# Performance work log

Measured on AMD Instinct MI355X. Metric: run time of the kernel, lower is better.

## Reference

```python
import jax, jax.numpy as jnp
import numpy as np

D_MODEL = 256
N_HEADS = 8
HEAD_DIM = D_MODEL // N_HEADS  # 32
N_LEVELS = 4
N_POINTS = 4
LEVEL_SHAPES = [(100, 100), (50, 50), (25, 25), (13, 13)]
LEVEL_STARTS = [0] + list(np.cumsum([h * w for h, w in LEVEL_SHAPES]))[:-1]
LEN_IN = int(sum(h * w for h, w in LEVEL_SHAPES))  # 13294
BATCH = 2
LEN_Q = LEN_IN  # encoder self-attention


def _offset_bias():
    # faithful to MSDeformAttn._reset_parameters for sampling_offsets bias
    thetas = np.arange(N_HEADS, dtype=np.float32) * (2.0 * np.pi / N_HEADS)
    grid = np.stack([np.cos(thetas), np.sin(thetas)], -1)
    grid = grid / np.abs(grid).max(-1, keepdims=True)
    grid = np.tile(grid.reshape(N_HEADS, 1, 1, 2), (1, N_LEVELS, N_POINTS, 1))
    for i in range(N_POINTS):
        grid[:, :, i, :] *= i + 1
    return jnp.asarray(grid.reshape(-1), dtype=jnp.float32)


def setup_inputs() -> dict:
    key = jax.random.key(0)
    ks = jax.random.split(key, 10)
    s = 1.0 / np.sqrt(D_MODEL)
    inp = {
        "query": jax.random.normal(ks[0], (BATCH, LEN_Q, D_MODEL), jnp.float32),
        "reference_points": jax.random.uniform(ks[1], (BATCH, LEN_Q, N_LEVELS, 2), jnp.float32),
        "input_flatten": jax.random.normal(ks[2], (BATCH, LEN_IN, D_MODEL), jnp.float32),
        "input_spatial_shapes": jnp.asarray(LEVEL_SHAPES, dtype=jnp.int32),
        "W_value": jax.random.normal(ks[3], (D_MODEL, D_MODEL), jnp.float32) * s,
        "b_value": jnp.zeros((D_MODEL,), jnp.float32),
        "W_off": jax.random.normal(ks[4], (D_MODEL, N_HEADS * N_LEVELS * N_POINTS * 2), jnp.float32) * 0.01,
        "b_off": _offset_bias(),
        "W_attn": jax.random.normal(ks[5], (D_MODEL, N_HEADS * N_LEVELS * N_POINTS), jnp.float32) * 0.01,
        "b_attn": jnp.zeros((N_HEADS * N_LEVELS * N_POINTS,), jnp.float32),
        "W_out": jax.random.normal(ks[6], (D_MODEL, D_MODEL), jnp.float32) * s,
        "b_out": jnp.zeros((D_MODEL,), jnp.float32),
    }
    return inp


def _corner(v_t, ix, iy, h, w):
    # v_t: (n, M, h*w, D); ix/iy: (n, M, LqP) int32. Zero padding outside.
    valid = (ix >= 0) & (ix < w) & (iy >= 0) & (iy < h)
    idx = jnp.clip(iy, 0, h - 1) * w + jnp.clip(ix, 0, w - 1)
    g = jnp.take_along_axis(v_t, idx[..., None], axis=2)  # (n, M, LqP, D)
    return g * valid[..., None].astype(v_t.dtype)


def _ms_deform_attn(query, reference_points, input_flatten,
                    W_value, b_value, W_off, b_off, W_attn, b_attn, W_out, b_out):
    n, lq, _ = query.shape
    value = (input_flatten @ W_value + b_value).reshape(n, LEN_IN, N_HEADS, HEAD_DIM)
    offs = (query @ W_off + b_off).reshape(n, lq, N_HEADS, N_LEVELS, N_POINTS, 2)
    aw = jax.nn.softmax(
        (query @ W_attn + b_attn).reshape(n, lq, N_HEADS, N_LEVELS * N_POINTS), axis=-1
    ).reshape(n, lq, N_HEADS, N_LEVELS, N_POINTS)
    # offset_normalizer = (w, h) per level
    norm = jnp.asarray([[w, h] for h, w in LEVEL_SHAPES], dtype=query.dtype)
    loc = reference_points[:, :, None, :, None, :] + offs / norm[None, None, None, :, None, :]

    acc = jnp.zeros((n, N_HEADS, lq, HEAD_DIM), dtype=value.dtype)
    for l, (h, w) in enumerate(LEVEL_SHAPES):
        s0 = LEVEL_STARTS[l]
        v_t = jnp.transpose(value[:, s0:s0 + h * w], (0, 2, 1, 3))  # (n, M, hw, D)
        ll = loc[:, :, :, l]  # (n, lq, M, P, 2) in [0,1]
        # grid_sample bilinear, align_corners=False: pixel = coord*size - 0.5
        x = ll[..., 0] * w - 0.5
        y = ll[..., 1] * h - 0.5
        x0 = jnp.floor(x); y0 = jnp.floor(y)
        tx = x - x0; ty = y - y0
        ix0 = x0.astype(jnp.int32); iy0 = y0.astype(jnp.int32)
        flat = lambda a: jnp.transpose(a, (0, 2, 1, 3)).reshape(n, N_HEADS, lq * N_POINTS)
        ix0f, iy0f = flat(ix0), flat(iy0)
        txf = flat(tx)[..., None]; tyf = flat(ty)[..., None]
        g00 = _corner(v_t, ix0f, iy0f, h, w)
        g01 = _corner(v_t, ix0f + 1, iy0f, h, w)
        g10 = _corner(v_t, ix0f, iy0f + 1, h, w)
        g11 = _corner(v_t, ix0f + 1, iy0f + 1, h, w)
        samp = (g00 * (1 - txf) * (1 - tyf) + g01 * txf * (1 - tyf)
                + g10 * (1 - txf) * tyf + g11 * txf * tyf)
        samp = samp.reshape(n, N_HEADS, lq, N_POINTS, HEAD_DIM)
        wl = jnp.transpose(aw[:, :, :, l], (0, 2, 1, 3))[..., None]  # (n, M, lq, P, 1)
        acc = acc + (samp * wl).sum(axis=3)

    out = jnp.transpose(acc, (0, 2, 1, 3)).reshape(n, lq, D_MODEL)
    return out @ W_out + b_out


def reference(query, reference_points, input_flatten, input_spatial_shapes,
              W_value, b_value, W_off, b_off, W_attn, b_attn, W_out, b_out):
    # input_spatial_shapes carried for signature fidelity; level geometry is static.
    return _ms_deform_attn(query, reference_points, input_flatten,
                           W_value, b_value, W_off, b_off, W_attn, b_attn, W_out, b_out)
```

## Files before the change

kernel.cpp:

```cpp
#include <hip/hip_runtime.h>

#define NH 8
#define HD 32
#define NL 4
#define NP 4
#define DM 256
#define LEN_IN_C 13294
#define LQ_C 13294
#define B_C 2
#define M_TOTAL (B_C * LQ_C)
#define MT_TILES 1662
#define RT32_TILES 831
#define GQ 32
#define QBLKS 831

typedef __attribute__((ext_vector_type(8))) short short8;
typedef __attribute__((ext_vector_type(4))) float floatx4;

__device__ __forceinline__ unsigned short f2bf(float x) {
    union { float f; unsigned int u; } a; a.f = x;
    unsigned int r = (a.u + 0x7FFFu + ((a.u >> 16) & 1u)) >> 16;
    return (unsigned short)r;
}
__device__ __forceinline__ unsigned short f2h(float x) {
    unsigned int r;
    asm("v_cvt_f16_f32 %0, %1" : "=v"(r) : "v"(x));
    return (unsigned short)r;
}
__device__ __forceinline__ unsigned int cvtpk_bf16(float lo, float hi) {
    unsigned int r;
    asm("v_cvt_pk_bf16_f32 %0, %1, %2" : "=v"(r) : "v"(lo), "v"(hi));
    return r;
}

#define FMAMIX_LO(acc, v, w) \
    asm("v_fma_mix_f32 %0, %1, %2, %0 op_sel_hi:[1,0,0]" : "+v"(acc) : "v"(v), "v"(w))
#define FMAMIX_HI(acc, v, w) \
    asm("v_fma_mix_f32 %0, %1, %2, %0 op_sel:[1,0,0] op_sel_hi:[1,0,0]" : "+v"(acc) : "v"(v), "v"(w))

__device__ __forceinline__ void conv_b_body(const float* __restrict__ W,
                                            unsigned short* __restrict__ Bsw,
                                            int Nsrc, int NTsrc, int NTtotal, int ntOff,
                                            int vblk) {
    const int u = vblk * 256 + threadIdx.x;
    const int lane = u & 63;
    const int unit = u >> 6;
    const int ntl = unit % NTsrc;
    const int kc = unit / NTsrc;
    const int n = ntl * 16 + (lane & 15);
    const int k0 = kc * 32 + (lane >> 4) * 8;
    short8 v;
#pragma unroll
    for (int j = 0; j < 8; ++j)
        v[j] = (short)f2bf(W[(size_t)(k0 + j) * Nsrc + n]);
    ((short8*)Bsw)[(size_t)(kc * NTtotal + ntOff + ntl) * 64 + lane] = v;
}

__global__ __launch_bounds__(256) void conv_weights_kernel(const float* __restrict__ Wv,
                                                           const float* __restrict__ Woff,
                                                           const float* __restrict__ Wattn,
                                                           const float* __restrict__ Wout,
                                                           const float* __restrict__ boff,
                                                           const float* __restrict__ battn,
                                                           unsigned short* __restrict__ BswV,
                                                           unsigned short* __restrict__ BswOA,
                                                           unsigned short* __restrict__ BswO,
                                                           float* __restrict__ fbias,
                                                           unsigned short* __restrict__ value,
                                                           unsigned short* __restrict__ AccSw) {
    const int blk = blockIdx.x;
    if (blk < 32)        conv_b_body(Wv,    BswV,  256, 16, 16, 0,  blk);
    else if (blk < 64)   conv_b_body(Woff,  BswOA, 256, 16, 24, 0,  blk - 32);
    else if (blk < 80)   conv_b_body(Wattn, BswOA, 128,  8, 24, 16, blk - 64);
    else if (blk < 112)  conv_b_body(Wout,  BswO,  256, 16, 16, 0,  blk - 80);
    else if (blk < 114) {
        const int t = (blk - 112) * 256 + threadIdx.x;
        if (t < 384) fbias[t] = (t < 256) ? boff[t] : battn[t - 256];
        else if (t < 416) {
            const int j = t - 384;
            value[-32 + j] = 0;
            value[(size_t)M_TOTAL * 256 + j] = 0;
        }
    } else {
        const int idx = threadIdx.x;
        if (idx < 128) {
            const int kc = idx >> 4;
            const int sub = idx & 15;
            const int lane = (12 + (sub & 3)) + 16 * (sub >> 2);
            const size_t unit = (size_t)(1661 * 8 + kc) * 64 + lane;
            short8 z = (short8){0, 0, 0, 0, 0, 0, 0, 0};
            ((short8*)AccSw)[unit] = z;
        }
    }
}

template <int NT, int OUTMODE>
__device__ __forceinline__ void gemm_lds_pipe(unsigned short* __restrict__ sA,
                                              const float* __restrict__ A,
                                              const unsigned short* __restrict__ Bsw,
                                              const float* __restrict__ bias,
                                              void* __restrict__ Cout, int M, int rt32) {
    constexpr int NTW = NT / 4;
    const int tid = threadIdx.x;
    const int lane = tid & 63;
    const int wave = tid >> 6;
    const int trow = rt32 * 32;

#pragma unroll
    for (int i = 0; i < 8; ++i) {
        const int li = i * 1024 + tid * 4;
        const int lrow = li >> 8;
        const int lcol = li & 255;
        const int srow = min(trow + lrow, M - 1);
        const float4 f = *(const float4*)(A + (size_t)srow * 256 + lcol);
        uint2 pk;
        pk.x = cvtpk_bf16(f.x, f.y);
        pk.y = cvtpk_bf16(f.z, f.w);
        const int lb = (li * 2) ^ ((lrow & 7) << 4);
        *(uint2*)((char*)sA + lb) = pk;
    }
    __syncthreads();

    const int m = lane & 15;
    const int q = lane >> 4;
    const short8* Bu = (const short8*)Bsw;
    const int swz = (m & 7) << 4;

    floatx4 acc[2][NTW];
#pragma unroll
    for (int r = 0; r < 2; ++r)
#pragma unroll
        for (int t = 0; t < NTW; ++t) acc[r][t] = (floatx4){0.f, 0.f, 0.f, 0.f};

    short8 br[2][NTW];
    short8 ar[2][2];
#pragma unroll
    for (int t = 0; t < NTW; ++t)
        br[0][t] = Bu[(size_t)(0 * NT + wave * NTW + t) * 64 + lane];
    ar[0][0] = *(const short8*)((const char*)sA + ((m * 512 + 0 * 64 + q * 16) ^ swz));
    ar[0][1] = *(const short8*)((const char*)sA + (((m + 16) * 512 + 0 * 64 + q * 16) ^ swz));

#pragma unroll
    for (int kc = 0; kc < 8; ++kc) {
        const int cur = kc & 1;
        const int nxt = cur ^ 1;
        if (kc < 7) {
#pragma unroll
            for (int t = 0; t < NTW; ++t)
                br[nxt][t] = Bu[(size_t)((kc + 1) * NT + wave * NTW + t) * 64 + lane];
            ar[nxt][0] = *(const short8*)((const char*)sA + ((m * 512 + (kc + 1) * 64 + q * 16) ^ swz));
            ar[nxt][1] = *(const short8*)((const char*)sA + (((m + 16) * 512 + (kc + 1) * 64 + q * 16) ^ swz));
        }
#pragma unroll
        for (int t = 0; t < NTW; ++t) {
            acc[0][t] = __builtin_amdgcn_mfma_f32_16x16x32_bf16(ar[cur][0], br[cur][t], acc[0][t], 0, 0, 0);
            acc[1][t] = __builtin_amdgcn_mfma_f32_16x16x32_bf16(ar[cur][1], br[cur][t], acc[1][t], 0, 0, 0);
        }
    }

    const int N = NT * 16;
    const int colq = lane & 15;
    const int rowq = (lane >> 4) * 4;
#pragma unroll
    for (int t = 0; t < NTW; ++t) {
        const int col = (wave * NTW + t) * 16 + colq;
        const float bc = bias[col];
#pragma unroll
        for (int r = 0; r < 2; ++r) {
#pragma unroll
            for (int reg = 0; reg < 4; ++reg) {
                const int row = trow + r * 16 + rowq + reg;
                if (row < M) {
                    const float v = acc[r][t][reg] + bc;
                    if (OUTMODE == 1) {
                        const int bb = row >= LEN_IN_C;
                        const int pos = row - (bb ? LEN_IN_C : 0);
                        const int hh = col >> 5;
                        const int dd = col & 31;
                        ((unsigned short*)Cout)[((size_t)((bb << 3) + hh) * LEN_IN_C + pos) * 32 + dd] = f2h(v);
                    } else {
                        ((float*)Cout)[(size_t)row * N + col] = v;
                    }
                }
            }
        }
    }
}

__global__ __launch_bounds__(256) void front_gemm_kernel(const float* __restrict__ inflat,
                                                         const float* __restrict__ query,
                                                         const unsigned short* __restrict__ BswV,
                                                         const unsigned short* __restrict__ BswOA,
                                                         const float* __restrict__ bv,
                                                         const float* __restrict__ fbias,
                                                         unsigned short* __restrict__ value,
                                                         float* __restrict__ fused, int M) {
    __shared__ unsigned short sA[32 * 256];
    const int x = blockIdx.x;
    const int rt32 = x >> 1;
    if ((x & 1) == 0)
        gemm_lds_pipe<16, 1>(sA, inflat, BswV, bv, (void*)value, M, rt32);
    else
        gemm_lds_pipe<24, 0>(sA, query, BswOA, fbias, (void*)fused, M, rt32);
}

__global__ __launch_bounds__(256) void back_gemm_kernel(const unsigned short* __restrict__ Asw,
                                                        const unsigned short* __restrict__ Bsw,
                                                        const float* __restrict__ bias,
                                                        float* __restrict__ Cout, int M) {
    constexpr int NT = 16;
    constexpr int NTW = 4;
    const int tid = threadIdx.x;
    const int lane = tid & 63;
    const int wave = tid >> 6;
    const int rt0 = blockIdx.x * 2;

    const short8* Au = (const short8*)Asw;
    const short8* Bu = (const short8*)Bsw;

    floatx4 acc[2][NTW];
#pragma unroll
    for (int r = 0; r < 2; ++r)
#pragma unroll
        for (int t = 0; t < NTW; ++t) acc[r][t] = (floatx4){0.f, 0.f, 0.f, 0.f};

    short8 br[2][NTW];
    short8 ar[2][2];
#pragma unroll
    for (int t = 0; t < NTW; ++t)
        br[0][t] = Bu[(size_t)(0 * NT + wave * NTW + t) * 64 + lane];
    ar[0][0] = Au[(size_t)(rt0 * 8 + 0) * 64 + lane];
    ar[0][1] = Au[(size_t)((rt0 + 1) * 8 + 0) * 64 + lane];

#pragma unroll
    for (int kc = 0; kc < 8; ++kc) {
        const int cur = kc & 1;
        const int nxt = cur ^ 1;
        if (kc < 7) {
#pragma unroll
            for (int t = 0; t < NTW; ++t)
                br[nxt][t] = Bu[(size_t)((kc + 1) * NT + wave * NTW + t) * 64 + lane];
            ar[nxt][0] = Au[(size_t)(rt0 * 8 + kc + 1) * 64 + lane];
            ar[nxt][1] = Au[(size_t)((rt0 + 1) * 8 + kc + 1) * 64 + lane];
        }
#pragma unroll
        for (int t = 0; t < NTW; ++t) {
            acc[0][t] = __builtin_amdgcn_mfma_f32_16x16x32_bf16(ar[cur][0], br[cur][t], acc[0][t], 0, 0, 0);
            acc[1][t] = __builtin_amdgcn_mfma_f32_16x16x32_bf16(ar[cur][1], br[cur][t], acc[1][t], 0, 0, 0);
        }
    }

    const int colq = lane & 15;
    const int rowq = (lane >> 4) * 4;
#pragma unroll
    for (int t = 0; t < NTW; ++t) {
        const int col = (wave * NTW + t) * 16 + colq;
        const float bc = bias[col];
#pragma unroll
        for (int r = 0; r < 2; ++r) {
#pragma unroll
            for (int reg = 0; reg < 4; ++reg) {
                const int row = (rt0 + r) * 16 + rowq + reg;
                if (row < M)
                    Cout[(size_t)row * 256 + col] = acc[r][t][reg] + bc;
            }
        }
    }
}

__global__ __launch_bounds__(256, 4) void msda_sample_kernel(const float* __restrict__ refp,
                                                             const unsigned short* __restrict__ value,
                                                             const float* __restrict__ fused,
                                                             unsigned short* __restrict__ AccSw) {
    constexpr int lvl_hw[4] = {100, 50, 25, 13};
    constexpr int lvl_s[4] = {0, 10000, 12500, 13125};

    const int wg = blockIdx.x;
    const int h = wg & 7;
    const int q0 = (wg >> 3) * GQ;
    const int tid = threadIdx.x;

    __shared__ float s_ref[GQ * 8];
    __shared__ uint4 s_pd[2][GQ * 17];

    s_ref[tid] = refp[min(q0 * 8 + tid, M_TOTAL * 8 - 1)];
    __syncthreads();

#pragma unroll
    for (int jj = 0; jj < 2; ++jj) {
        const int job = jj * 256 + tid;
        const int qq = job >> 4;
        const int t16 = job & 15;
        const int l = t16 >> 2;
        const int bq = min(q0 + qq, M_TOTAL - 1);
        const int b = (bq >= LQ_C) ? 1 : 0;

        const float logit = fused[(size_t)bq * 384 + 256 + h * 16 + t16];
        float m = logit;
#pragma unroll
        for (int mask = 1; mask < 16; mask <<= 1) m = fmaxf(m, __shfl_xor(m, mask));
        const float e = expf(logit - m);
        float s = e;
#pragma unroll
        for (int mask = 1; mask < 16; mask <<= 1) s += __shfl_xor(s, mask);
        const float aw = e / s;

        const int whl = lvl_hw[l];
        const float fwh = (float)whl;
        const float2 oxy = *(const float2*)(fused + (size_t)bq * 384 + (h * 16 + t16) * 2);
        const float x = s_ref[qq * 8 + l * 2] * fwh + oxy.x - 0.5f;
        const float y = s_ref[qq * 8 + l * 2 + 1] * fwh + oxy.y - 0.5f;
        const float x0f = floorf(x), y0f = floorf(y);
        const float tx = x - x0f, ty = y - y0f;
        const int ix0 = (int)x0f, iy0 = (int)y0f;

        const bool xv0 = (unsigned)ix0 < (unsigned)whl;
        const bool xv1 = (unsigned)(ix0 + 1) < (unsigned)whl;
        const bool yv0 = (unsigned)iy0 < (unsigned)whl;
        const bool yv1 = (unsigned)(iy0 + 1) < (unsigned)whl;

        const int cxp = min(max(ix0, -1), whl - 1);
        const int cy0 = min(max(iy0, 0), whl - 1);
        const int cy1 = min(max(iy0 + 1, 0), whl - 1);

        const int posb = (b * 8 + h) * LEN_IN_C + lvl_s[l];
        const int offT = (posb + cy0 * whl + cxp) * 64;
        const int offB = (posb + cy1 * whl + cxp) * 64;
        const float w00 = (xv0 && yv0) ? aw * (1.f - tx) * (1.f - ty) : 0.f;
        const float w01 = (xv1 && yv0) ? aw * tx * (1.f - ty) : 0.f;
        const float w10 = (xv0 && yv1) ? aw * (1.f - tx) * ty : 0.f;
        const float w11 = (xv1 && yv1) ? aw * tx * ty : 0.f;
        const int slot = qq * 17 + t16;
        uint4 d0, d1;
        d0.x = (unsigned)offT; d0.y = (unsigned)offB;
        d0.z = __float_as_uint(w00); d0.w = __float_as_uint(w10);
        d1.x = (unsigned)offT; d1.y = (unsigned)offB;
        d1.z = __float_as_uint(w01); d1.w = __float_as_uint(w11);
        s_pd[0][slot] = d0;
        s_pd[1][slot] = d1;
    }
    __syncthreads();

    const int qq = tid >> 3;
    const int l8 = tid & 7;
    const char* vbp = (const char*)value + l8 * 16;
    const int side = (l8 >> 2) & 1;
    const uint4* pd = &s_pd[side][qq * 17];

    uint4 dsc[2][4];
    uint4 vt[2][4], vb[2][4];
#pragma unroll
    for (int j = 0; j < 4; ++j) dsc[0][j] = pd[j];
#pragma unroll
    for (int j = 0; j < 4; ++j) {
        vt[0][j] = *(const uint4*)(vbp + (int)dsc[0][j].x);
        vb[0][j] = *(const uint4*)(vbp + (int)dsc[0][j].y);
    }

    float a0 = 0.f, a1 = 0.f, a2 = 0.f, a3 = 0.f;
    float a4 = 0.f, a5 = 0.f, a6 = 0.f, a7 = 0.f;
#pragma unroll
    for (int c = 0; c < 4; ++c) {
        const int cur = c & 1;
        const int nxt = cur ^ 1;
        if (c < 3) {
#pragma unroll
            for (int j = 0; j < 4; ++j) dsc[nxt][j] = pd[(c + 1) * 4 + j];
#pragma unroll
            for (int j = 0; j < 4; ++j) {
                vt[nxt][j] = *(const uint4*)(vbp + (int)dsc[nxt][j].x);
                vb[nxt][j] = *(const uint4*)(vbp + (int)dsc[nxt][j].y);
            }
        }
#pragma unroll
        for (int j = 0; j < 4; ++j) {
            const float wt = __uint_as_float(dsc[cur][j].z);
            const float wb = __uint_as_float(dsc[cur][j].w);
            const uint4 t4 = vt[cur][j];
            const uint4 b4 = vb[cur][j];
            FMAMIX_LO(a0, t4.x, wt); FMAMIX_HI(a1, t4.x, wt);
            FMAMIX_LO(a2, t4.y, wt); FMAMIX_HI(a3, t4.y, wt);
            FMAMIX_LO(a4, t4.z, wt); FMAMIX_HI(a5, t4.z, wt);
            FMAMIX_LO(a6, t4.w, wt); FMAMIX_HI(a7, t4.w, wt);
            FMAMIX_LO(a0, b4.x, wb); FMAMIX_HI(a1, b4.x, wb);
            FMAMIX_LO(a2, b4.y, wb); FMAMIX_HI(a3, b4.y, wb);
            FMAMIX_LO(a4, b4.z, wb); FMAMIX_HI(a5, b4.z, wb);
            FMAMIX_LO(a6, b4.w, wb); FMAMIX_HI(a7, b4.w, wb);
        }
    }

    a0 += __shfl_xor(a0, 4); a1 += __shfl_xor(a1, 4);
    a2 += __shfl_xor(a2, 4); a3 += __shfl_xor(a3, 4);
    a4 += __shfl_xor(a4, 4); a5 += __shfl_xor(a5, 4);
    a6 += __shfl_xor(a6, 4); a7 += __shfl_xor(a7, 4);

    const int bq = q0 + qq;
    if (side == 0 && bq < M_TOTAL) {
        const int rt = bq >> 4, mm = bq & 15;
        const int unit = (rt * 8 + h) * 64 + ((l8 & 3) * 16 + mm);
        uint4 o;
        o.x = cvtpk_bf16(a0, a1);
        o.y = cvtpk_bf16(a2, a3);
        o.z = cvtpk_bf16(a4, a5);
        o.w = cvtpk_bf16(a6, a7);
        *(uint4*)(AccSw + (size_t)unit * 8) = o;
    }
}

extern "C" void kernel_launch(void* const* d_in, const int* in_sizes, int n_in,
                              void* d_out, int out_size, void* d_ws, size_t ws_size,
                              hipStream_t stream) {
    const float* query  = (const float*)d_in[0];
    const float* refp   = (const float*)d_in[1];
    const float* inflat = (const float*)d_in[2];
    const float* Wv    = (const float*)d_in[4];
    const float* bv    = (const float*)d_in[5];
    const float* Woff  = (const float*)d_in[6];
    const float* boff  = (const float*)d_in[7];
    const float* Wattn = (const float*)d_in[8];
    const float* battn = (const float*)d_in[9];
    const float* Wout  = (const float*)d_in[10];
    const float* bout  = (const float*)d_in[11];
    float* out = (float*)d_out;

    char* p = (char*)d_ws;
    unsigned short* AccSw = (unsigned short*)p;
    p += (size_t)MT_TILES * 8 * 64 * 8 * sizeof(unsigned short);
    unsigned short* BswV = (unsigned short*)p;   p += (size_t)8 * 16 * 64 * 8 * 2;
    unsigned short* BswOA = (unsigned short*)p;  p += (size_t)8 * 24 * 64 * 8 * 2;
    unsigned short* BswO = (unsigned short*)p;   p += (size_t)8 * 16 * 64 * 8 * 2;
    float* fbias = (float*)p;                    p += 384 * sizeof(float);
    unsigned short* value = (unsigned short*)p + 32;
    p += ((size_t)M_TOTAL * 256 + 64) * sizeof(unsigned short);
    float* fused = (float*)p;                    p += (size_t)M_TOTAL * 384 * 4;

    const int M = M_TOTAL;

    conv_weights_kernel<<<115, 256, 0, stream>>>(Wv, Woff, Wattn, Wout, boff, battn,
                                                 BswV, BswOA, BswO, fbias, value, AccSw);
    front_gemm_kernel<<<RT32_TILES * 2, 256, 0, stream>>>(inflat, query, BswV, BswOA,
                                                          bv, fbias, value, fused, M);
    msda_sample_kernel<<<QBLKS * 8, 256, 0, stream>>>(refp, value, fused, AccSw);
    back_gemm_kernel<<<RT32_TILES, 256, 0, stream>>>(AccSw, BswO, bout, out, M);
}
```

Measured before the change: 198.3 us.

## Make front and back GEMMs persistent with double-buffered prefetch

Both projection GEMMs become persistent grids of 512 blocks that loop over row tiles. The front GEMM double-buffers its LDS staging so the next tile's global loads overlap the current tile's MFMA work. The back GEMM loads the whole weight fragment into registers once per block and ping-pongs A fragments for 16-row tiles. This removes per-tile launch and weight reload cost, at the price of higher register pressure and fewer blocks to hide latency.

Result: slower. 255.4 us (+28.8%).

```diff
diff --git a/kernel.cpp b/kernel.cpp
--- a/kernel.cpp
+++ b/kernel.cpp
@@ -13,6 +13,9 @@
 #define RT32_TILES 831
 #define GQ 32
 #define QBLKS 831
+#define FRONT_BLOCKS 512
+#define FRONT_STRIDE 256
+#define BACK_BLOCKS 512
 
 typedef __attribute__((ext_vector_type(8))) short short8;
 typedef __attribute__((ext_vector_type(4))) float floatx4;
@@ -94,37 +97,42 @@
     }
 }
 
-template <int NT, int OUTMODE>
-__device__ __forceinline__ void gemm_lds_pipe(unsigned short* __restrict__ sA,
-                                              const float* __restrict__ A,
-                                              const unsigned short* __restrict__ Bsw,
-                                              const float* __restrict__ bias,
-                                              void* __restrict__ Cout, int M, int rt32) {
-    constexpr int NTW = NT / 4;
-    const int tid = threadIdx.x;
-    const int lane = tid & 63;
-    const int wave = tid >> 6;
-    const int trow = rt32 * 32;
-
+__device__ __forceinline__ void stage_load(float4 (&stg)[8], const float* __restrict__ A,
+                                           int trow, int M, int tid) {
 #pragma unroll
     for (int i = 0; i < 8; ++i) {
         const int li = i * 1024 + tid * 4;
         const int lrow = li >> 8;
         const int lcol = li & 255;
         const int srow = min(trow + lrow, M - 1);
-        const float4 f = *(const float4*)(A + (size_t)srow * 256 + lcol);
+        stg[i] = *(const float4*)(A + (size_t)srow * 256 + lcol);
+    }
+}
+
+__device__ __forceinline__ void stage_write(unsigned short* sbuf, const float4 (&stg)[8], int tid) {
+#pragma unroll
+    for (int i = 0; i < 8; ++i) {
+        const int li = i * 1024 + tid * 4;
+        const int lrow = li >> 8;
         uint2 pk;
-        pk.x = cvtpk_bf16(f.x, f.y);
-        pk.y = cvtpk_bf16(f.z, f.w);
-        const int lb = (li * 2) ^ ((lrow & 7) << 4);
-        *(uint2*)((char*)sA + lb) = pk;
-    }
-    __syncthreads();
-
+        pk.x = cvtpk_bf16(stg[i].x, stg[i].y);
+        pk.y = cvtpk_bf16(stg[i].z, stg[i].w);
+        *(uint2*)((char*)sbuf + ((li * 2) ^ ((lrow & 7) << 4))) = pk;
+    }
+}
+
+template <int NT, int OUTMODE>
+__device__ __forceinline__ void tile_compute(const unsigned short* sbuf,
+                                             const unsigned short* __restrict__ Bsw,
+                                             const float* __restrict__ bias,
+                                             void* __restrict__ Cout, int M, int rt32,
+                                             int lane, int wave) {
+    constexpr int NTW = NT / 4;
     const int m = lane & 15;
     const int q = lane >> 4;
     const short8* Bu = (const short8*)Bsw;
     const int swz = (m & 7) << 4;
+    const int trow = rt32 * 32;
 
     floatx4 acc[2][NTW];
 #pragma unroll
@@ -137,8 +145,8 @@
 #pragma unroll
     for (int t = 0; t < NTW; ++t)
         br[0][t] = Bu[(size_t)(0 * NT + wave * NTW + t) * 64 + lane];
-    ar[0][0] = *(const short8*)((const char*)sA + ((m * 512 + 0 * 64 + q * 16) ^ swz));
-    ar[0][1] = *(const short8*)((const char*)sA + (((m + 16) * 512 + 0 * 64 + q * 16) ^ swz));
+    ar[0][0] = *(const short8*)((const char*)sbuf + ((m * 512 + 0 * 64 + q * 16) ^ swz));
+    ar[0][1] = *(const short8*)((const char*)sbuf + (((m + 16) * 512 + 0 * 64 + q * 16) ^ swz));
 
 #pragma unroll
     for (int kc = 0; kc < 8; ++kc) {
@@ -148,8 +156,8 @@
 #pragma unroll
             for (int t = 0; t < NTW; ++t)
                 br[nxt][t] = Bu[(size_t)((kc + 1) * NT + wave * NTW + t) * 64 + lane];
-            ar[nxt][0] = *(const short8*)((const char*)sA + ((m * 512 + (kc + 1) * 64 + q * 16) ^ swz));
-            ar[nxt][1] = *(const short8*)((const char*)sA + (((m + 16) * 512 + (kc + 1) * 64 + q * 16) ^ swz));
+            ar[nxt][0] = *(const short8*)((const char*)sbuf + ((m * 512 + (kc + 1) * 64 + q * 16) ^ swz));
+            ar[nxt][1] = *(const short8*)((const char*)sbuf + (((m + 16) * 512 + (kc + 1) * 64 + q * 16) ^ swz));
         }
 #pragma unroll
         for (int t = 0; t < NTW; ++t) {
@@ -187,84 +195,107 @@
     }
 }
 
-__global__ __launch_bounds__(256) void front_gemm_kernel(const float* __restrict__ inflat,
-                                                         const float* __restrict__ query,
-                                                         const unsigned short* __restrict__ BswV,
-                                                         const unsigned short* __restrict__ BswOA,
-                                                         const float* __restrict__ bv,
-                                                         const float* __restrict__ fbias,
-                                                         unsigned short* __restrict__ value,
-                                                         float* __restrict__ fused, int M) {
-    __shared__ unsigned short sA[32 * 256];
-    const int x = blockIdx.x;
-    const int rt32 = x >> 1;
-    if ((x & 1) == 0)
-        gemm_lds_pipe<16, 1>(sA, inflat, BswV, bv, (void*)value, M, rt32);
-    else
-        gemm_lds_pipe<24, 0>(sA, query, BswOA, fbias, (void*)fused, M, rt32);
-}
-
-__global__ __launch_bounds__(256) void back_gemm_kernel(const unsigned short* __restrict__ Asw,
-                                                        const unsigned short* __restrict__ Bsw,
-                                                        const float* __restrict__ bias,
-                                                        float* __restrict__ Cout, int M) {
-    constexpr int NT = 16;
-    constexpr int NTW = 4;
+__global__ __launch_bounds__(256, 2) void front_gemm_kernel(const float* __restrict__ inflat,
+                                                            const float* __restrict__ query,
+                                                            const unsigned short* __restrict__ BswV,
+                                                            const unsigned short* __restrict__ BswOA,
+                                                            const float* __restrict__ bv,
+                                                            const float* __restrict__ fbias,
+                                                            unsigned short* __restrict__ value,
+                                                            float* __restrict__ fused, int M) {
+    __shared__ unsigned short sA[2][32 * 256];
     const int tid = threadIdx.x;
     const int lane = tid & 63;
     const int wave = tid >> 6;
-    const int rt0 = blockIdx.x * 2;
-
+    const int flavor = blockIdx.x & 1;
+    const int rt0 = blockIdx.x >> 1;
+    const float* A = flavor ? query : inflat;
+
+    float4 stg[8];
+    stage_load(stg, A, rt0 * 32, M, tid);
+    stage_write(sA[0], stg, tid);
+
+    int cur = 0;
+    for (int rt = rt0; rt < RT32_TILES; rt += FRONT_STRIDE) {
+        __syncthreads();
+        const int rtn = rt + FRONT_STRIDE;
+        if (rtn < RT32_TILES) stage_load(stg, A, rtn * 32, M, tid);
+        if (flavor == 0)
+            tile_compute<16, 1>(sA[cur], BswV, bv, (void*)value, M, rt, lane, wave);
+        else
+            tile_compute<24, 0>(sA[cur], BswOA, fbias, (void*)fused, M, rt, lane, wave);
+        if (rtn < RT32_TILES) stage_write(sA[cur ^ 1], stg, tid);
+        cur ^= 1;
+    }
+}
+
+__device__ __forceinline__ void back_loadA(short8 (&ar)[8], const short8* __restrict__ Au,
+                                           int rt, int lane) {
+#pragma unroll
+    for (int kc = 0; kc < 8; ++kc)
+        ar[kc] = Au[(size_t)(rt * 8 + kc) * 64 + lane];
+}
+
+__device__ __forceinline__ void back_compute(const short8 (&ar)[8], const short8 (&br)[8][4],
+                                             const float* __restrict__ bias,
+                                             float* __restrict__ Cout, int M, int rt,
+                                             int lane, int wave) {
+    floatx4 acc[4];
+#pragma unroll
+    for (int t = 0; t < 4; ++t) acc[t] = (floatx4){0.f, 0.f, 0.f, 0.f};
+#pragma unroll
+    for (int kc = 0; kc < 8; ++kc)
+#pragma unroll
+        for (int t = 0; t < 4; ++t)
+            acc[t] = __builtin_amdgcn_mfma_f32_16x16x32_bf16(ar[kc], br[kc][t], acc[t], 0, 0, 0);
+
+    const int colq = lane & 15;
+    const int rowq = (lane >> 4) * 4;
+#pragma unroll
+    for (int t = 0; t < 4; ++t) {
+        const int col = (wave * 4 + t) * 16 + colq;
+        const float bc = bias[col];
+#pragma unroll
+        for (int reg = 0; reg < 4; ++reg) {
+            const int row = rt * 16 + rowq + reg;
+            if (row < M)
+                Cout[(size_t)row * 256 + col] = acc[t][reg] + bc;
+        }
+    }
+}
+
+__global__ __launch_bounds__(256, 2) void back_gemm_kernel(const unsigned short* __restrict__ Asw,
+                                                           const unsigned short* __restrict__ Bsw,
+                                                           const float* __restrict__ bias,
+                                                           float* __restrict__ Cout, int M) {
+    const int tid = threadIdx.x;
+    const int lane = tid & 63;
+    const int wave = tid >> 6;
     const short8* Au = (const short8*)Asw;
     const short8* Bu = (const short8*)Bsw;
 
-    floatx4 acc[2][NTW];
-#pragma unroll
-    for (int r = 0; r < 2; ++r)
-#pragma unroll
-        for (int t = 0; t < NTW; ++t) acc[r][t] = (floatx4){0.f, 0.f, 0.f, 0.f};
-
-    short8 br[2][NTW];
-    short8 ar[2][2];
-#pragma unroll
-    for (int t = 0; t < NTW; ++t)
-        br[0][t] = Bu[(size_t)(0 * NT + wave * NTW + t) * 64 + lane];
-    ar[0][0] = Au[(size_t)(rt0 * 8 + 0) * 64 + lane];
-    ar[0][1] = Au[(size_t)((rt0 + 1) * 8 + 0) * 64 + lane];
-
-#pragma unroll
-    for (int kc = 0; kc < 8; ++kc) {
-        const int cur = kc & 1;
-        const int nxt = cur ^ 1;
-        if (kc < 7) {
-#pragma unroll
-            for (int t = 0; t < NTW; ++t)
-                br[nxt][t] = Bu[(size_t)((kc + 1) * NT + wave * NTW + t) * 64 + lane];
-            ar[nxt][0] = Au[(size_t)(rt0 * 8 + kc + 1) * 64 + lane];
-            ar[nxt][1] = Au[(size_t)((rt0 + 1) * 8 + kc + 1) * 64 + lane];
-        }
-#pragma unroll
-        for (int t = 0; t < NTW; ++t) {
-            acc[0][t] = __builtin_amdgcn_mfma_f32_16x16x32_bf16(ar[cur][0], br[cur][t], acc[0][t], 0, 0, 0);
-            acc[1][t] = __builtin_amdgcn_mfma_f32_16x16x32_bf16(ar[cur][1], br[cur][t], acc[1][t], 0, 0, 0);
-        }
-    }
-
-    const int colq = lane & 15;
-    const int rowq = (lane >> 4) * 4;
-#pragma unroll
-    for (int t = 0; t < NTW; ++t) {
-        const int col = (wave * NTW + t) * 16 + colq;
-        const float bc = bias[col];
-#pragma unroll
-        for (int r = 0; r < 2; ++r) {
-#pragma unroll
-            for (int reg = 0; reg < 4; ++reg) {
-                const int row = (rt0 + r) * 16 + rowq + reg;
-                if (row < M)
-                    Cout[(size_t)row * 256 + col] = acc[r][t][reg] + bc;
-            }
-        }
+    short8 br[8][4];
+#pragma unroll
+    for (int kc = 0; kc < 8; ++kc)
+#pragma unroll
+        for (int t = 0; t < 4; ++t)
+            br[kc][t] = Bu[(size_t)(kc * 16 + wave * 4 + t) * 64 + lane];
+
+    short8 arA[8], arB[8];
+    int rt = blockIdx.x;
+    if (rt >= MT_TILES) return;
+    back_loadA(arA, Au, rt, lane);
+    while (true) {
+        int rtn = rt + BACK_BLOCKS;
+        if (rtn < MT_TILES) back_loadA(arB, Au, rtn, lane);
+        back_compute(arA, br, bias, Cout, M, rt, lane, wave);
+        rt = rtn;
+        if (rt >= MT_TILES) break;
+        rtn = rt + BACK_BLOCKS;
+        if (rtn < MT_TILES) back_loadA(arA, Au, rtn, lane);
+        back_compute(arB, br, bias, Cout, M, rt, lane, wave);
+        rt = rtn;
+        if (rt >= MT_TILES) break;
     }
 }
 
@@ -438,8 +469,8 @@
 
     conv_weights_kernel<<<115, 256, 0, stream>>>(Wv, Woff, Wattn, Wout, boff, battn,
                                                  BswV, BswOA, BswO, fbias, value, AccSw);
-    front_gemm_kernel<<<RT32_TILES * 2, 256, 0, stream>>>(inflat, query, BswV, BswOA,
-                                                          bv, fbias, value, fused, M);
+    front_gemm_kernel<<<FRONT_BLOCKS, 256, 0, stream>>>(inflat, query, BswV, BswOA,
+                                                        bv, fbias, value, fused, M);
     msda_sample_kernel<<<QBLKS * 8, 256, 0, stream>>>(refp, value, fused, AccSw);
-    back_gemm_kernel<<<RT32_TILES, 256, 0, stream>>>(AccSw, BswO, bout, out, M);
-}
+    back_gemm_kernel<<<BACK_BLOCKS, 256, 0, stream>>>(AccSw, BswO, bout, out, M);
+}
```

## Stage fp32 A tiles via direct global-to-LDS loads and convert at fragment read

Applied to the files above, without the earlier changes.

The front GEMM no longer loads A through registers and packs it to bf16 in swizzled LDS. It now issues global_load_lds DMA of fp32 rows into padded LDS (row stride 1040 bytes) and converts to bf16 when the MFMA fragments are read. Both front and back GEMMs also drop the explicit register double-buffering of A/B fragments in favour of a plain loop unrolled by 2. This cuts VGPR staging and load instructions, but doubles LDS footprint and traffic and moves the conversion work into the inner loop.

Result: faster. 189.2 us (-4.6%).

```diff
diff --git a/kernel.cpp b/kernel.cpp
--- a/kernel.cpp
+++ b/kernel.cpp
@@ -13,6 +13,7 @@
 #define RT32_TILES 831
 #define GQ 32
 #define QBLKS 831
+#define LROWB 1040
 
 typedef __attribute__((ext_vector_type(8))) short short8;
 typedef __attribute__((ext_vector_type(4))) float floatx4;
@@ -37,6 +38,12 @@
     asm("v_fma_mix_f32 %0, %1, %2, %0 op_sel_hi:[1,0,0]" : "+v"(acc) : "v"(v), "v"(w))
 #define FMAMIX_HI(acc, v, w) \
     asm("v_fma_mix_f32 %0, %1, %2, %0 op_sel:[1,0,0] op_sel_hi:[1,0,0]" : "+v"(acc) : "v"(v), "v"(w))
+
+__device__ __forceinline__ void dma16(const float* g, float* l) {
+    __builtin_amdgcn_global_load_lds(
+        (const __attribute__((address_space(1))) unsigned int*)(g),
+        (__attribute__((address_space(3))) unsigned int*)(l), 16, 0, 0);
+}
 
 __device__ __forceinline__ void conv_b_body(const float* __restrict__ W,
                                             unsigned short* __restrict__ Bsw,
@@ -95,36 +102,15 @@
 }
 
 template <int NT, int OUTMODE>
-__device__ __forceinline__ void gemm_lds_pipe(unsigned short* __restrict__ sA,
-                                              const float* __restrict__ A,
-                                              const unsigned short* __restrict__ Bsw,
-                                              const float* __restrict__ bias,
-                                              void* __restrict__ Cout, int M, int rt32) {
+__device__ __forceinline__ void tile_compute_f32lds(const float* __restrict__ sA,
+                                                    const unsigned short* __restrict__ Bsw,
+                                                    const float* __restrict__ bias,
+                                                    void* __restrict__ Cout, int M, int trow,
+                                                    int lane, int wave) {
     constexpr int NTW = NT / 4;
-    const int tid = threadIdx.x;
-    const int lane = tid & 63;
-    const int wave = tid >> 6;
-    const int trow = rt32 * 32;
-
-#pragma unroll
-    for (int i = 0; i < 8; ++i) {
-        const int li = i * 1024 + tid * 4;
-        const int lrow = li >> 8;
-        const int lcol = li & 255;
-        const int srow = min(trow + lrow, M - 1);
-        const float4 f = *(const float4*)(A + (size_t)srow * 256 + lcol);
-        uint2 pk;
-        pk.x = cvtpk_bf16(f.x, f.y);
-        pk.y = cvtpk_bf16(f.z, f.w);
-        const int lb = (li * 2) ^ ((lrow & 7) << 4);
-        *(uint2*)((char*)sA + lb) = pk;
-    }
-    __syncthreads();
-
     const int m = lane & 15;
     const int q = lane >> 4;
     const short8* Bu = (const short8*)Bsw;
-    const int swz = (m & 7) << 4;
 
     floatx4 acc[2][NTW];
 #pragma unroll
@@ -132,29 +118,24 @@
 #pragma unroll
         for (int t = 0; t < NTW; ++t) acc[r][t] = (floatx4){0.f, 0.f, 0.f, 0.f};
 
-    short8 br[2][NTW];
-    short8 ar[2][2];
-#pragma unroll
-    for (int t = 0; t < NTW; ++t)
-        br[0][t] = Bu[(size_t)(0 * NT + wave * NTW + t) * 64 + lane];
-    ar[0][0] = *(const short8*)((const char*)sA + ((m * 512 + 0 * 64 + q * 16) ^ swz));
-    ar[0][1] = *(const short8*)((const char*)sA + (((m + 16) * 512 + 0 * 64 + q * 16) ^ swz));
-
-#pragma unroll
+#pragma unroll 2
     for (int kc = 0; kc < 8; ++kc) {
-        const int cur = kc & 1;
-        const int nxt = cur ^ 1;
-        if (kc < 7) {
-#pragma unroll
-            for (int t = 0; t < NTW; ++t)
-                br[nxt][t] = Bu[(size_t)((kc + 1) * NT + wave * NTW + t) * 64 + lane];
-            ar[nxt][0] = *(const short8*)((const char*)sA + ((m * 512 + (kc + 1) * 64 + q * 16) ^ swz));
-            ar[nxt][1] = *(const short8*)((const char*)sA + (((m + 16) * 512 + (kc + 1) * 64 + q * 16) ^ swz));
+        short8 a[2];
+#pragma unroll
+        for (int r = 0; r < 2; ++r) {
+            const char* fb = (const char*)sA + (m + r * 16) * LROWB + kc * 128 + q * 32;
+            const float4 f0 = *(const float4*)fb;
+            const float4 f1 = *(const float4*)(fb + 16);
+            union { uint4 u; short8 s; } c;
+            c.u.x = cvtpk_bf16(f0.x, f0.y); c.u.y = cvtpk_bf16(f0.z, f0.w);
+            c.u.z = cvtpk_bf16(f1.x, f1.y); c.u.w = cvtpk_bf16(f1.z, f1.w);
+            a[r] = c.s;
         }
 #pragma unroll
         for (int t = 0; t < NTW; ++t) {
-            acc[0][t] = __builtin_amdgcn_mfma_f32_16x16x32_bf16(ar[cur][0], br[cur][t], acc[0][t], 0, 0, 0);
-            acc[1][t] = __builtin_amdgcn_mfma_f32_16x16x32_bf16(ar[cur][1], br[cur][t], acc[1][t], 0, 0, 0);
+            const short8 b = Bu[(size_t)(kc * NT + wave * NTW + t) * 64 + lane];
+            acc[0][t] = __builtin_amdgcn_mfma_f32_16x16x32_bf16(a[0], b, acc[0][t], 0, 0, 0);
+            acc[1][t] = __builtin_amdgcn_mfma_f32_16x16x32_bf16(a[1], b, acc[1][t], 0, 0, 0);
         }
     }
 
@@ -195,13 +176,28 @@
                                                          const float* __restrict__ fbias,
                                                          unsigned short* __restrict__ value,
                                                          float* __restrict__ fused, int M) {
-    __shared__ unsigned short sA[32 * 256];
+    __shared__ float sA[32 * LROWB / 4];
+    const int tid = threadIdx.x;
+    const int lane = tid & 63;
+    const int wave = tid >> 6;
     const int x = blockIdx.x;
-    const int rt32 = x >> 1;
-    if ((x & 1) == 0)
-        gemm_lds_pipe<16, 1>(sA, inflat, BswV, bv, (void*)value, M, rt32);
+    const int flavor = x & 1;
+    const int trow = (x >> 1) * 32;
+    const float* A = flavor ? query : inflat;
+
+#pragma unroll
+    for (int i = 0; i < 8; ++i) {
+        const int lrow = i * 4 + wave;
+        const int srow = min(trow + lrow, M - 1);
+        dma16(A + (size_t)srow * 256 + lane * 4,
+              (float*)((char*)sA + lrow * LROWB));
+    }
+    __syncthreads();
+
+    if (flavor == 0)
+        tile_compute_f32lds<16, 1>(sA, BswV, bv, (void*)value, M, trow, lane, wave);
     else
-        gemm_lds_pipe<24, 0>(sA, query, BswOA, fbias, (void*)fused, M, rt32);
+        tile_compute_f32lds<24, 0>(sA, BswOA, fbias, (void*)fused, M, trow, lane, wave);
 }
 
 __global__ __launch_bounds__(256) void back_gemm_kernel(const unsigned short* __restrict__ Asw,
@@ -224,29 +220,15 @@
 #pragma unroll
         for (int t = 0; t < NTW; ++t) acc[r][t] = (floatx4){0.f, 0.f, 0.f, 0.f};
 
-    short8 br[2][NTW];
-    short8 ar[2][2];
-#pragma unroll
-    for (int t = 0; t < NTW; ++t)
-        br[0][t] = Bu[(size_t)(0 * NT + wave * NTW + t) * 64 + lane];
-    ar[0][0] = Au[(size_t)(rt0 * 8 + 0) * 64 + lane];
-    ar[0][1] = Au[(size_t)((rt0 + 1) * 8 + 0) * 64 + lane];
-
-#pragma unroll
+#pragma unroll 2
     for (int kc = 0; kc < 8; ++kc) {
-        const int cur = kc & 1;
-        const int nxt = cur ^ 1;
-        if (kc < 7) {
-#pragma unroll
-            for (int t = 0; t < NTW; ++t)
-                br[nxt][t] = Bu[(size_t)((kc + 1) * NT + wave * NTW + t) * 64 + lane];
-            ar[nxt][0] = Au[(size_t)(rt0 * 8 + kc + 1) * 64 + lane];
-            ar[nxt][1] = Au[(size_t)((rt0 + 1) * 8 + kc + 1) * 64 + lane];
-        }
+        const short8 a0 = Au[(size_t)(rt0 * 8 + kc) * 64 + lane];
+        const short8 a1 = Au[(size_t)((rt0 + 1) * 8 + kc) * 64 + lane];
 #pragma unroll
         for (int t = 0; t < NTW; ++t) {
-            acc[0][t] = __builtin_amdgcn_mfma_f32_16x16x32_bf16(ar[cur][0], br[cur][t], acc[0][t], 0, 0, 0);
-            acc[1][t] = __builtin_amdgcn_mfma_f32_16x16x32_bf16(ar[cur][1], br[cur][t], acc[1][t], 0, 0, 0);
+            const short8 b = Bu[(size_t)(kc * NT + wave * NTW + t) * 64 + lane];
+            acc[0][t] = __builtin_amdgcn_mfma_f32_16x16x32_bf16(a0, b, acc[0][t], 0, 0, 0);
+            acc[1][t] = __builtin_amdgcn_mfma_f32_16x16x32_bf16(a1, b, acc[1][t], 0, 0, 0);
         }
     }
 
```
